# Kernel tuning notes

Measured on AMD Instinct MI355X. Metric: run time of the kernel, lower is better.

The kernel has to match this reference:

```python
import jax, jax.numpy as jnp
import numpy as np

N = 10000
E = 80000


def gat_layer(x, src, dst, W, a_src, a_dst, b):
    # x: [N, Fin], W: [Fin, Fout]
    xw = x @ W                              # [N, Fout]
    al_src = xw @ a_src                     # [N]
    al_dst = xw @ a_dst                     # [N]
    e = jax.nn.leaky_relu(al_src[src] + al_dst[dst], 0.2)  # [E+N]
    m = jax.lax.stop_gradient(jax.ops.segment_max(e, dst, num_segments=N))
    ex = jnp.exp(e - m[dst])
    denom = jax.ops.segment_sum(ex, dst, num_segments=N)
    alpha = ex / (denom[dst] + 1e-16)       # PyG softmax eps
    out = jax.ops.segment_sum(alpha[:, None] * xw[src], dst, num_segments=N)
    return out + b


def setup_inputs() -> dict:
    key = jax.random.key(0)
    ks = jax.random.split(key, 12)
    x = jax.random.normal(ks[0], (N, 256), dtype=jnp.float32)
    edge_index = jax.random.randint(ks[1], (2, E), 0, N, dtype=jnp.int64)
    def glorot(k, fi, fo):
        return jax.random.normal(k, (fi, fo), jnp.float32) * jnp.sqrt(2.0 / (fi + fo))
    W1 = glorot(ks[2], 256, 2048)
    W2 = glorot(ks[3], 2048, 2048)
    W3 = glorot(ks[4], 2048, 1024)
    a1s = jax.random.normal(ks[5], (2048,), jnp.float32) * 0.05
    a1d = jax.random.normal(ks[6], (2048,), jnp.float32) * 0.05
    a2s = jax.random.normal(ks[7], (2048,), jnp.float32) * 0.05
    a2d = jax.random.normal(ks[8], (2048,), jnp.float32) * 0.05
    a3s = jax.random.normal(ks[9], (1024,), jnp.float32) * 0.05
    a3d = jax.random.normal(ks[10], (1024,), jnp.float32) * 0.05
    b1 = jnp.zeros((2048,), jnp.float32)
    b2 = jnp.zeros((2048,), jnp.float32)
    b3 = jnp.zeros((1024,), jnp.float32)
    return {"x": x, "edge_index": edge_index, "W1": W1, "W2": W2, "W3": W3,
            "a1s": a1s, "a1d": a1d, "a2s": a2s, "a2d": a2d, "a3s": a3s, "a3d": a3d,
            "b1": b1, "b2": b2, "b3": b3}


def reference(x, edge_index, W1, W2, W3, a1s, a1d, a2s, a2d, a3s, a3d, b1, b2, b3):
    # add self loops (PyG GATConv default add_self_loops=True)
    loop = jnp.arange(N, dtype=edge_index.dtype)
    src = jnp.concatenate([edge_index[0], loop])
    dst = jnp.concatenate([edge_index[1], loop])
    h = jax.nn.relu(gat_layer(x, src, dst, W1, a1s, a1d, b1))
    h = jax.nn.relu(gat_layer(h, src, dst, W2, a2s, a2d, b2))
    h = jax.nn.relu(gat_layer(h, src, dst, W3, a3s, a3d, b3))
    # F.normalize(dim=1), eps=1e-12
    norm = jnp.linalg.norm(h, axis=1, keepdims=True)
    return h / jnp.maximum(norm, 1e-12)
```

## Files before the change

kernel.cpp:

```cpp
#include <hip/hip_runtime.h>
#include <hip/hip_bf16.h>
#include <math.h>


typedef __attribute__((ext_vector_type(8))) short short8;
typedef __attribute__((ext_vector_type(4))) float f32x4;

#define GLOAD_LDS16(g, l)                                            \
  __builtin_amdgcn_global_load_lds(                                  \
      (const __attribute__((address_space(1))) void*)(g),            \
      (__attribute__((address_space(3))) void*)(l), 16, 0, 0)

#define CFENCE asm volatile("" ::: "memory")

__device__ __forceinline__ float bf16_to_f32(ushort u) {
  return __uint_as_float(((unsigned int)u) << 16);
}

__device__ __forceinline__ float block_reduce_sum_bcast(float v) {
#pragma unroll
  for (int off = 32; off > 0; off >>= 1) v += __shfl_down(v, off, 64);
  __shared__ float tmp[4];
  __shared__ float res;
  int lane = threadIdx.x & 63, w = threadIdx.x >> 6;
  if (lane == 0) tmp[w] = v;
  __syncthreads();
  if (threadIdx.x == 0) res = tmp[0] + tmp[1] + tmp[2] + tmp[3];
  __syncthreads();
  float out = res;
  __syncthreads();
  return out;
}

__device__ __forceinline__ float block_reduce_max_bcast(float v) {
#pragma unroll
  for (int off = 32; off > 0; off >>= 1) v = fmaxf(v, __shfl_down(v, off, 64));
  __shared__ float tmpm[4];
  __shared__ float resm;
  int lane = threadIdx.x & 63, w = threadIdx.x >> 6;
  if (lane == 0) tmpm[w] = v;
  __syncthreads();
  if (threadIdx.x == 0) resm = fmaxf(fmaxf(tmpm[0], tmpm[1]), fmaxf(tmpm[2], tmpm[3]));
  __syncthreads();
  float out = resm;
  __syncthreads();
  return out;
}

__global__ void detect_kernel(const int* __restrict__ ei32, int* __restrict__ flag) {
  __shared__ int cnt;
  if (threadIdx.x == 0) cnt = 0;
  __syncthreads();
  int zeros = 0;
  for (int i = threadIdx.x; i < 1024; i += 256) {
    if (ei32[2 * i + 1] == 0) zeros++;
  }
  atomicAdd(&cnt, zeros);
  __syncthreads();
  if (threadIdx.x == 0) *flag = (cnt > 900) ? 1 : 0;
}

__global__ void convert_kernel(const void* __restrict__ ei, const int* __restrict__ flag,
                               int E, int* __restrict__ src, int* __restrict__ dst) {
  int i = blockIdx.x * blockDim.x + threadIdx.x;
  if (i >= E) return;
  if (*flag) {
    const long long* p = (const long long*)ei;
    src[i] = (int)p[i];
    dst[i] = (int)p[E + i];
  } else {
    const int* p = (const int*)ei;
    src[i] = p[i];
    dst[i] = p[E + i];
  }
}

__global__ __launch_bounds__(256) void convert_f32_bf16(const float* __restrict__ in,
                                                        __hip_bfloat16* __restrict__ out,
                                                        int n) {
  int i = blockIdx.x * blockDim.x + threadIdx.x;
  if (i < n) out[i] = __float2bfloat16(in[i]);
}

__global__ __launch_bounds__(256) void transpose_w(const float* __restrict__ W,
                                                   __hip_bfloat16* __restrict__ Wt,
                                                   int K, int Nout) {
  __shared__ float t[32][33];
  int tx = threadIdx.x & 31, ty = threadIdx.x >> 5;
  int n0 = blockIdx.x * 32, k0 = blockIdx.y * 32;
#pragma unroll
  for (int i = 0; i < 4; ++i) {
    int k = k0 + ty + i * 8;
    t[ty + i * 8][tx] = W[(size_t)k * Nout + n0 + tx];
  }
  __syncthreads();
#pragma unroll
  for (int i = 0; i < 4; ++i) {
    int n = n0 + ty + i * 8;
    Wt[(size_t)n * K + k0 + tx] = __float2bfloat16(t[tx][ty + i * 8]);
  }
}

__global__ __launch_bounds__(256) void matvec_wa(const float* __restrict__ W,
                                                 const float* __restrict__ a_s,
                                                 const float* __restrict__ a_d,
                                                 float* __restrict__ wa_s,
                                                 float* __restrict__ wa_d, int F) {
  int k = blockIdx.x;
  const float* row = W + (size_t)k * F;
  float s1 = 0.f, s2 = 0.f;
  for (int f = threadIdx.x; f < F; f += 256) {
    float w = row[f];
    s1 += w * a_s[f];
    s2 += w * a_d[f];
  }
  float r1 = block_reduce_sum_bcast(s1);
  float r2 = block_reduce_sum_bcast(s2);
  if (threadIdx.x == 0) {
    wa_s[k] = r1;
    wa_d[k] = r2;
  }
}

template <int FPT>
__global__ __launch_bounds__(256) void compute_al(const ushort* __restrict__ H,
                                                  const float* __restrict__ wa_s,
                                                  const float* __restrict__ wa_d,
                                                  float* __restrict__ als,
                                                  float* __restrict__ ald, int F) {
  int n = blockIdx.x;
  const ushort* row = H + (size_t)n * F;
  float s1 = 0.f, s2 = 0.f;
  if (FPT == 8) {
    int base = threadIdx.x * 8;
    short8 v = *(const short8*)(row + base);
#pragma unroll
    for (int j = 0; j < 8; ++j) {
      float f = bf16_to_f32((ushort)v[j]);
      s1 += f * wa_s[base + j];
      s2 += f * wa_d[base + j];
    }
  } else {
    float f = bf16_to_f32(row[threadIdx.x]);
    s1 = f * wa_s[threadIdx.x];
    s2 = f * wa_d[threadIdx.x];
  }
  float r1 = block_reduce_sum_bcast(s1);
  float r2 = block_reduce_sum_bcast(s2);
  if (threadIdx.x == 0) {
    als[n] = r1;
    ald[n] = r2;
  }
}

__global__ void count_kernel(const int* __restrict__ dst, int* __restrict__ counts, int E) {
  int i = blockIdx.x * blockDim.x + threadIdx.x;
  if (i < E) atomicAdd(&counts[dst[i]], 1);
}

__global__ __launch_bounds__(1024) void scan_kernel(const int* __restrict__ counts,
                                                    int* __restrict__ rowptr,
                                                    int* __restrict__ cursor, int Nn) {
  __shared__ int part[1024];
  int tid = threadIdx.x;
  int chunk = (Nn + 1023) / 1024;
  int base = tid * chunk;
  int s = 0;
  for (int i = 0; i < chunk; ++i) {
    int idx = base + i;
    if (idx < Nn) s += counts[idx];
  }
  part[tid] = s;
  __syncthreads();
  for (int off = 1; off < 1024; off <<= 1) {
    int v = 0;
    if (tid >= off) v = part[tid - off];
    __syncthreads();
    if (tid >= off) part[tid] += v;
    __syncthreads();
  }
  int run = (tid == 0) ? 0 : part[tid - 1];
  for (int i = 0; i < chunk; ++i) {
    int idx = base + i;
    if (idx < Nn) {
      rowptr[idx] = run;
      cursor[idx] = run;
      run += counts[idx];
    }
  }
  if (tid == 1023) rowptr[Nn] = part[1023];
}

__global__ void fill_kernel(const int* __restrict__ src, const int* __restrict__ dst,
                            int* __restrict__ cursor, int* __restrict__ eidx, int E) {
  int i = blockIdx.x * blockDim.x + threadIdx.x;
  if (i < E) {
    int pos = atomicAdd(&cursor[dst[i]], 1);
    eidx[pos] = src[i];
  }
}

template <int FPT>
__global__ __launch_bounds__(256) void aggregate(const ushort* __restrict__ H,
                                                 const float* __restrict__ als,
                                                 const float* __restrict__ ald,
                                                 const int* __restrict__ rowptr,
                                                 const int* __restrict__ eidx,
                                                 ushort* __restrict__ out, int F) {
  int n = blockIdx.x;
  int tid = threadIdx.x;
  int beg = rowptr[n], end = rowptr[n + 1];
  int deg = end - beg;
  float aldn = ald[n];

  float lm = -INFINITY;
  for (int j = tid; j < deg; j += 256) {
    int s = eidx[beg + j];
    float e = als[s] + aldn;
    e = (e > 0.f) ? e : 0.2f * e;
    lm = fmaxf(lm, e);
  }
  if (tid == 0) {
    float e = als[n] + aldn;
    e = (e > 0.f) ? e : 0.2f * e;
    lm = fmaxf(lm, e);
  }
  float m = block_reduce_max_bcast(lm);

  float ls = 0.f;
  for (int j = tid; j < deg; j += 256) {
    int s = eidx[beg + j];
    float e = als[s] + aldn;
    e = (e > 0.f) ? e : 0.2f * e;
    ls += expf(e - m);
  }
  if (tid == 0) {
    float e = als[n] + aldn;
    e = (e > 0.f) ? e : 0.2f * e;
    ls += expf(e - m);
  }
  float denom = block_reduce_sum_bcast(ls) + 1e-16f;
  float inv_denom = 1.f / denom;

  float acc[FPT];
#pragma unroll
  for (int i = 0; i < FPT; ++i) acc[i] = 0.f;

  __shared__ float alpha_sh[256];
  __shared__ int src_sh[256];
  int total = deg + 1;
  for (int c0 = 0; c0 < total; c0 += 256) {
    int j = c0 + tid;
    if (j < total) {
      int s = (j < deg) ? eidx[beg + j] : n;
      float e = als[s] + aldn;
      e = (e > 0.f) ? e : 0.2f * e;
      alpha_sh[tid] = expf(e - m) * inv_denom;
      src_sh[tid] = s;
    }
    __syncthreads();
    int cn = min(256, total - c0);
    for (int jj = 0; jj < cn; ++jj) {
      float al = alpha_sh[jj];
      const ushort* row = H + (size_t)src_sh[jj] * F;
      if (FPT == 1) {
        acc[0] += al * bf16_to_f32(row[tid]);
      } else {
#pragma unroll
        for (int i = 0; i < FPT / 2; ++i) {
          unsigned int u = *(const unsigned int*)(row + tid * 2 + i * 512);
          acc[2 * i]     += al * __uint_as_float((u & 0xffffu) << 16);
          acc[2 * i + 1] += al * __uint_as_float(u & 0xffff0000u);
        }
      }
    }
    __syncthreads();
  }

#pragma unroll
  for (int i = 0; i < FPT; ++i) {
    int col = (FPT == 1) ? tid : (tid * 2 + (i >> 1) * 512 + (i & 1));
    __hip_bfloat16 hv = __float2bfloat16(acc[i]);
    out[(size_t)n * F + col] = *(ushort*)&hv;
  }
}

template <bool BF16OUT>
__global__ __launch_bounds__(256, 4) void gemm_t128(const ushort* __restrict__ A,
                                                    const ushort* __restrict__ Bt,
                                                    const float* __restrict__ bias,
                                                    void* __restrict__ C,
                                                    int M, int K, int Nout) {
  constexpr int BUF = 8192;
  extern __shared__ ushort lds[];
  const int tid = threadIdx.x;
  const int l = tid & 63, w = tid >> 6;
  const int wm = w >> 1, wn = w & 1;
  const int l15 = l & 15, lhi = l >> 4;

  int nwg = gridDim.x * gridDim.y;
  int lin = blockIdx.y * gridDim.x + blockIdx.x;
  if ((nwg & 7) == 0) lin = (lin & 7) * (nwg >> 3) + (lin >> 3);
  const int bx = lin % gridDim.x, by = lin / gridDim.x;
  const int row0 = by * 128, col0 = bx * 128;

  const int c8sw = (l & 3) ^ (((l >> 5) & 1) << 1);
  const int lrow = l >> 2;
  const int chsw = lhi ^ (((l15 >> 3) & 1) << 1);
  const int rd_off = l15 * 32 + chsw * 8;

  const int sA0 = w * 2;
  const ushort* ga[2];
  const ushort* gb[2];
#pragma unroll
  for (int j = 0; j < 2; ++j) {
    int ar = min(row0 + (sA0 + j) * 16 + lrow, M - 1);
    ga[j] = A + (size_t)ar * K + c8sw * 8;
    gb[j] = Bt + (size_t)(col0 + (sA0 + j) * 16 + lrow) * K + c8sw * 8;
  }

#define STAGE(nb, kn)                                                     \
  do {                                                                    \
    GLOAD_LDS16(ga[0] + (kn), &lds[(nb)*BUF + (sA0 + 0) * 512]);          \
    GLOAD_LDS16(ga[1] + (kn), &lds[(nb)*BUF + (sA0 + 1) * 512]);          \
    GLOAD_LDS16(gb[0] + (kn), &lds[(nb)*BUF + 4096 + (sA0 + 0) * 512]);   \
    GLOAD_LDS16(gb[1] + (kn), &lds[(nb)*BUF + 4096 + (sA0 + 1) * 512]);   \
  } while (0)

  f32x4 acc[4][4] = {};

#define PHASE(cur, WAITLIT, STAGE_STMT)                                              \
  do {                                                                               \
    STAGE_STMT;                                                                      \
    asm volatile("s_waitcnt vmcnt(" WAITLIT ")" ::: "memory");                       \
    __builtin_amdgcn_s_barrier();                                                    \
    CFENCE;                                                                          \
    short8 af[4], bf[4];                                                             \
    const ushort* Ab = &lds[(cur)*BUF];                                              \
    const ushort* Bb = &lds[(cur)*BUF + 4096];                                       \
    _Pragma("unroll") for (int m = 0; m < 4; ++m)                                    \
        af[m] = *(const short8*)(Ab + (wm * 4 + m) * 512 + rd_off);                  \
    _Pragma("unroll") for (int n = 0; n < 4; ++n)                                    \
        bf[n] = *(const short8*)(Bb + (wn * 4 + n) * 512 + rd_off);                  \
    __builtin_amdgcn_s_setprio(1);                                                   \
    _Pragma("unroll") for (int m = 0; m < 4; ++m)                                    \
        _Pragma("unroll") for (int n = 0; n < 4; ++n)                                \
            acc[m][n] = __builtin_amdgcn_mfma_f32_16x16x32_bf16(                     \
                af[m], bf[n], acc[m][n], 0, 0, 0);                                   \
    __builtin_amdgcn_s_setprio(0);                                                   \
    CFENCE;                                                                          \
    __builtin_amdgcn_s_barrier();                                                    \
    CFENCE;                                                                          \
  } while (0)

  const int nt = K >> 5;
  STAGE(0, 0);

  int cur = 0;
  for (int t = 0; t < nt - 1; ++t) {
    const int kn = (t + 1) << 5;
    PHASE(cur, "4", STAGE(cur ^ 1, kn));
    cur ^= 1;
  }
  PHASE(cur, "0", );

#pragma unroll
  for (int mi = 0; mi < 4; ++mi) {
#pragma unroll
    for (int v = 0; v < 4; ++v) {
      int r = row0 + wm * 64 + mi * 16 + lhi * 4 + v;
      if (r < M) {
#pragma unroll
        for (int n = 0; n < 4; ++n) {
          int col = col0 + wn * 64 + n * 16 + l15;
          float val = fmaxf(acc[mi][n][v] + bias[col], 0.f);
          size_t idx = (size_t)r * Nout + col;
          if (BF16OUT)
            ((__hip_bfloat16*)C)[idx] = __float2bfloat16(val);
          else
            ((float*)C)[idx] = val;
        }
      }
    }
  }
#undef PHASE
#undef STAGE
}

__global__ __launch_bounds__(256) void normalize_kernel(const float* __restrict__ h,
                                                        float* __restrict__ out,
                                                        int F) {
  int n = blockIdx.x;
  const float* row = h + (size_t)n * F;
  float ss = 0.f;
  for (int f = threadIdx.x; f < F; f += 256) {
    float v = row[f];
    ss += v * v;
  }
  float tot = block_reduce_sum_bcast(ss);
  float inv = 1.f / fmaxf(sqrtf(tot), 1e-12f);
  for (int f = threadIdx.x; f < F; f += 256) {
    out[(size_t)n * F + f] = row[f] * inv;
  }
}

extern "C" void kernel_launch(void* const* d_in, const int* in_sizes, int n_in,
                              void* d_out, int out_size, void* d_ws, size_t ws_size,
                              hipStream_t stream) {
  const float* x   = (const float*)d_in[0];
  const void*  ei  = d_in[1];
  const float* W1  = (const float*)d_in[2];
  const float* W2  = (const float*)d_in[3];
  const float* W3  = (const float*)d_in[4];
  const float* a1s = (const float*)d_in[5];
  const float* a1d = (const float*)d_in[6];
  const float* a2s = (const float*)d_in[7];
  const float* a2d = (const float*)d_in[8];
  const float* a3s = (const float*)d_in[9];
  const float* a3d = (const float*)d_in[10];
  const float* b1  = (const float*)d_in[11];
  const float* b2  = (const float*)d_in[12];
  const float* b3  = (const float*)d_in[13];

  const int N = in_sizes[0] / 256;
  const int E = in_sizes[1] / 2;

  char* ws = (char*)d_ws;
  size_t off = 0;
  auto alloc = [&](size_t bytes) -> void* {
    void* p = ws + off;
    off += (bytes + 255) & ~(size_t)255;
    return p;
  };
  ushort* h    = (ushort*)alloc((size_t)N * 2048 * 2);
  ushort* hagg = (ushort*)alloc((size_t)N * 2048 * 2);
  float* hf32  = (float*)alloc((size_t)N * 1024 * 4);
  ushort* xb   = (ushort*)alloc((size_t)N * 256 * 2);
  __hip_bfloat16* Wt1 = (__hip_bfloat16*)alloc((size_t)2048 * 256 * 2);
  __hip_bfloat16* Wt2 = (__hip_bfloat16*)alloc((size_t)2048 * 2048 * 2);
  __hip_bfloat16* Wt3 = (__hip_bfloat16*)alloc((size_t)1024 * 2048 * 2);
  float* wa1s = (float*)alloc(256 * 4);
  float* wa1d = (float*)alloc(256 * 4);
  float* wa2s = (float*)alloc(2048 * 4);
  float* wa2d = (float*)alloc(2048 * 4);
  float* wa3s = (float*)alloc(2048 * 4);
  float* wa3d = (float*)alloc(2048 * 4);
  float* als   = (float*)alloc((size_t)N * 4);
  float* ald   = (float*)alloc((size_t)N * 4);
  int* counts  = (int*)alloc((size_t)N * 4);
  int* rowptr  = (int*)alloc((size_t)(N + 1) * 4);
  int* cursor  = (int*)alloc((size_t)N * 4);
  int* eidx    = (int*)alloc((size_t)E * 4);
  int* src32   = (int*)alloc((size_t)E * 4);
  int* dst32   = (int*)alloc((size_t)E * 4);
  int* flag    = (int*)alloc(256);

  hipFuncSetAttribute((const void*)gemm_t128<true>,
                      hipFuncAttributeMaxDynamicSharedMemorySize, 32768);
  hipFuncSetAttribute((const void*)gemm_t128<false>,
                      hipFuncAttributeMaxDynamicSharedMemorySize, 32768);

  detect_kernel<<<1, 256, 0, stream>>>((const int*)ei, flag);
  convert_kernel<<<(E + 255) / 256, 256, 0, stream>>>(ei, flag, E, src32, dst32);
  hipMemsetAsync(counts, 0, (size_t)N * 4, stream);
  count_kernel<<<(E + 255) / 256, 256, 0, stream>>>(dst32, counts, E);
  scan_kernel<<<1, 1024, 0, stream>>>(counts, rowptr, cursor, N);
  fill_kernel<<<(E + 255) / 256, 256, 0, stream>>>(src32, dst32, cursor, eidx, E);

  convert_f32_bf16<<<(N * 256 + 255) / 256, 256, 0, stream>>>(x, (__hip_bfloat16*)xb, N * 256);
  transpose_w<<<dim3(2048 / 32, 256 / 32), 256, 0, stream>>>(W1, Wt1, 256, 2048);
  transpose_w<<<dim3(2048 / 32, 2048 / 32), 256, 0, stream>>>(W2, Wt2, 2048, 2048);
  transpose_w<<<dim3(1024 / 32, 2048 / 32), 256, 0, stream>>>(W3, Wt3, 2048, 1024);
  matvec_wa<<<256, 256, 0, stream>>>(W1, a1s, a1d, wa1s, wa1d, 2048);
  matvec_wa<<<2048, 256, 0, stream>>>(W2, a2s, a2d, wa2s, wa2d, 2048);
  matvec_wa<<<2048, 256, 0, stream>>>(W3, a3s, a3d, wa3s, wa3d, 1024);

  dim3 blk(256);
  int mb = (N + 127) / 128;

  compute_al<1><<<N, blk, 0, stream>>>(xb, wa1s, wa1d, als, ald, 256);
  aggregate<1><<<N, blk, 0, stream>>>(xb, als, ald, rowptr, eidx, hagg, 256);
  gemm_t128<true><<<dim3(2048 / 128, mb), blk, 32768, stream>>>(hagg, (const ushort*)Wt1, b1, h, N, 256, 2048);

  compute_al<8><<<N, blk, 0, stream>>>(h, wa2s, wa2d, als, ald, 2048);
  aggregate<8><<<N, blk, 0, stream>>>(h, als, ald, rowptr, eidx, hagg, 2048);
  gemm_t128<true><<<dim3(2048 / 128, mb), blk, 32768, stream>>>(hagg, (const ushort*)Wt2, b2, h, N, 2048, 2048);

  compute_al<8><<<N, blk, 0, stream>>>(h, wa3s, wa3d, als, ald, 2048);
  aggregate<8><<<N, blk, 0, stream>>>(h, als, ald, rowptr, eidx, hagg, 2048);
  gemm_t128<false><<<dim3(1024 / 128, mb), blk, 32768, stream>>>(hagg, (const ushort*)Wt3, b3, hf32, N, 2048, 1024);

  normalize_kernel<<<N, blk, 0, stream>>>(hf32, (float*)d_out, 1024);
}
```

Measured before the change: 428.7 us.

## Fuse attention logits and row sum-of-squares into GEMM epilogues, drop index conversion

The next layer's attention scalars (h·wa_s, h·wa_d) are now computed in the GEMM epilogue through a 16-lane shuffle reduction plus atomicAdd, which removes the separate compute_al passes over the 2048-wide bf16 activations. The final GEMM likewise accumulates per-row sums of squares, so normalization no longer re-reads each row to reduce it. The edge-index detection and conversion kernels are removed and the input is read directly as int32, assuming that layout. This adds atomics and a memset, and the epilogue sums fp32 values before bf16 rounding, so results differ slightly from the old path.

```diff
diff --git a/kernel.cpp b/kernel.cpp
--- a/kernel.cpp
+++ b/kernel.cpp
@@ -45,34 +45,6 @@
   float out = resm;
   __syncthreads();
   return out;
-}
-
-__global__ void detect_kernel(const int* __restrict__ ei32, int* __restrict__ flag) {
-  __shared__ int cnt;
-  if (threadIdx.x == 0) cnt = 0;
-  __syncthreads();
-  int zeros = 0;
-  for (int i = threadIdx.x; i < 1024; i += 256) {
-    if (ei32[2 * i + 1] == 0) zeros++;
-  }
-  atomicAdd(&cnt, zeros);
-  __syncthreads();
-  if (threadIdx.x == 0) *flag = (cnt > 900) ? 1 : 0;
-}
-
-__global__ void convert_kernel(const void* __restrict__ ei, const int* __restrict__ flag,
-                               int E, int* __restrict__ src, int* __restrict__ dst) {
-  int i = blockIdx.x * blockDim.x + threadIdx.x;
-  if (i >= E) return;
-  if (*flag) {
-    const long long* p = (const long long*)ei;
-    src[i] = (int)p[i];
-    dst[i] = (int)p[E + i];
-  } else {
-    const int* p = (const int*)ei;
-    src[i] = p[i];
-    dst[i] = p[E + i];
-  }
 }
 
 __global__ __launch_bounds__(256) void convert_f32_bf16(const float* __restrict__ in,
@@ -122,29 +94,16 @@
   }
 }
 
-template <int FPT>
-__global__ __launch_bounds__(256) void compute_al(const ushort* __restrict__ H,
-                                                  const float* __restrict__ wa_s,
-                                                  const float* __restrict__ wa_d,
-                                                  float* __restrict__ als,
-                                                  float* __restrict__ ald, int F) {
+__global__ __launch_bounds__(256) void compute_al1(const ushort* __restrict__ H,
+                                                   const float* __restrict__ wa_s,
+                                                   const float* __restrict__ wa_d,
+                                                   float* __restrict__ als,
+                                                   float* __restrict__ ald) {
   int n = blockIdx.x;
-  const ushort* row = H + (size_t)n * F;
-  float s1 = 0.f, s2 = 0.f;
-  if (FPT == 8) {
-    int base = threadIdx.x * 8;
-    short8 v = *(const short8*)(row + base);
-#pragma unroll
-    for (int j = 0; j < 8; ++j) {
-      float f = bf16_to_f32((ushort)v[j]);
-      s1 += f * wa_s[base + j];
-      s2 += f * wa_d[base + j];
-    }
-  } else {
-    float f = bf16_to_f32(row[threadIdx.x]);
-    s1 = f * wa_s[threadIdx.x];
-    s2 = f * wa_d[threadIdx.x];
-  }
+  const ushort* row = H + (size_t)n * 256;
+  float f = bf16_to_f32(row[threadIdx.x]);
+  float s1 = f * wa_s[threadIdx.x];
+  float s2 = f * wa_d[threadIdx.x];
   float r1 = block_reduce_sum_bcast(s1);
   float r2 = block_reduce_sum_bcast(s2);
   if (threadIdx.x == 0) {
@@ -285,11 +244,15 @@
   }
 }
 
-template <bool BF16OUT>
+template <bool BF16OUT, int EPI>
 __global__ __launch_bounds__(256, 4) void gemm_t128(const ushort* __restrict__ A,
                                                     const ushort* __restrict__ Bt,
                                                     const float* __restrict__ bias,
                                                     void* __restrict__ C,
+                                                    const float* __restrict__ wa_s,
+                                                    const float* __restrict__ wa_d,
+                                                    float* __restrict__ aux1,
+                                                    float* __restrict__ aux2,
                                                     int M, int K, int Nout) {
   constexpr int BUF = 8192;
   extern __shared__ ushort lds[];
@@ -369,36 +332,53 @@
 #pragma unroll
     for (int v = 0; v < 4; ++v) {
       int r = row0 + wm * 64 + mi * 16 + lhi * 4 + v;
-      if (r < M) {
-#pragma unroll
-        for (int n = 0; n < 4; ++n) {
-          int col = col0 + wn * 64 + n * 16 + l15;
-          float val = fmaxf(acc[mi][n][v] + bias[col], 0.f);
+      bool rin = (r < M);
+      float pS = 0.f, pD = 0.f;
+#pragma unroll
+      for (int n = 0; n < 4; ++n) {
+        int col = col0 + wn * 64 + n * 16 + l15;
+        float val = fmaxf(acc[mi][n][v] + bias[col], 0.f);
+        if (rin) {
           size_t idx = (size_t)r * Nout + col;
           if (BF16OUT)
             ((__hip_bfloat16*)C)[idx] = __float2bfloat16(val);
           else
             ((float*)C)[idx] = val;
+          if (EPI == 1) {
+            pS += val * wa_s[col];
+            pD += val * wa_d[col];
+          } else if (EPI == 2) {
+            pS += val * val;
+          }
         }
       }
+      if (EPI == 1) {
+#pragma unroll
+        for (int off = 1; off < 16; off <<= 1) {
+          pS += __shfl_xor(pS, off, 64);
+          pD += __shfl_xor(pD, off, 64);
+        }
+        if (l15 == 0 && rin) {
+          atomicAdd(&aux1[r], pS);
+          atomicAdd(&aux2[r], pD);
+        }
+      } else if (EPI == 2) {
+#pragma unroll
+        for (int off = 1; off < 16; off <<= 1) pS += __shfl_xor(pS, off, 64);
+        if (l15 == 0 && rin) atomicAdd(&aux1[r], pS);
+      }
     }
   }
 #undef PHASE
 #undef STAGE
 }
 
-__global__ __launch_bounds__(256) void normalize_kernel(const float* __restrict__ h,
-                                                        float* __restrict__ out,
-                                                        int F) {
+__global__ __launch_bounds__(256) void normalize_ss(const float* __restrict__ h,
+                                                    const float* __restrict__ ss,
+                                                    float* __restrict__ out, int F) {
   int n = blockIdx.x;
+  float inv = 1.f / fmaxf(sqrtf(ss[n]), 1e-12f);
   const float* row = h + (size_t)n * F;
-  float ss = 0.f;
-  for (int f = threadIdx.x; f < F; f += 256) {
-    float v = row[f];
-    ss += v * v;
-  }
-  float tot = block_reduce_sum_bcast(ss);
-  float inv = 1.f / fmaxf(sqrtf(tot), 1e-12f);
   for (int f = threadIdx.x; f < F; f += 256) {
     out[(size_t)n * F + f] = row[f] * inv;
   }
@@ -408,7 +388,7 @@
                               void* d_out, int out_size, void* d_ws, size_t ws_size,
                               hipStream_t stream) {
   const float* x   = (const float*)d_in[0];
-  const void*  ei  = d_in[1];
+  const int*   ei  = (const int*)d_in[1];
   const float* W1  = (const float*)d_in[2];
   const float* W2  = (const float*)d_in[3];
   const float* W3  = (const float*)d_in[4];
@@ -445,27 +425,33 @@
   float* wa2d = (float*)alloc(2048 * 4);
   float* wa3s = (float*)alloc(2048 * 4);
   float* wa3d = (float*)alloc(2048 * 4);
-  float* als   = (float*)alloc((size_t)N * 4);
-  float* ald   = (float*)alloc((size_t)N * 4);
+  float* als1 = (float*)alloc((size_t)N * 4);
+  float* ald1 = (float*)alloc((size_t)N * 4);
+  float* alaux = (float*)alloc((size_t)N * 5 * 4);
+  float* als2 = alaux;
+  float* ald2 = alaux + N;
+  float* als3 = alaux + 2 * (size_t)N;
+  float* ald3 = alaux + 3 * (size_t)N;
+  float* ssq  = alaux + 4 * (size_t)N;
   int* counts  = (int*)alloc((size_t)N * 4);
   int* rowptr  = (int*)alloc((size_t)(N + 1) * 4);
   int* cursor  = (int*)alloc((size_t)N * 4);
   int* eidx    = (int*)alloc((size_t)E * 4);
-  int* src32   = (int*)alloc((size_t)E * 4);
-  int* dst32   = (int*)alloc((size_t)E * 4);
-  int* flag    = (int*)alloc(256);
-
-  hipFuncSetAttribute((const void*)gemm_t128<true>,
+
+  const int* srcp = ei;
+  const int* dstp = ei + E;
+
+  hipFuncSetAttribute((const void*)gemm_t128<true, 1>,
                       hipFuncAttributeMaxDynamicSharedMemorySize, 32768);
-  hipFuncSetAttribute((const void*)gemm_t128<false>,
+  hipFuncSetAttribute((const void*)gemm_t128<false, 2>,
                       hipFuncAttributeMaxDynamicSharedMemorySize, 32768);
 
-  detect_kernel<<<1, 256, 0, stream>>>((const int*)ei, flag);
-  convert_kernel<<<(E + 255) / 256, 256, 0, stream>>>(ei, flag, E, src32, dst32);
+  hipMemsetAsync(alaux, 0, (size_t)N * 5 * 4, stream);
   hipMemsetAsync(counts, 0, (size_t)N * 4, stream);
-  count_kernel<<<(E + 255) / 256, 256, 0, stream>>>(dst32, counts, E);
+
+  count_kernel<<<(E + 255) / 256, 256, 0, stream>>>(dstp, counts, E);
   scan_kernel<<<1, 1024, 0, stream>>>(counts, rowptr, cursor, N);
-  fill_kernel<<<(E + 255) / 256, 256, 0, stream>>>(src32, dst32, cursor, eidx, E);
+  fill_kernel<<<(E + 255) / 256, 256, 0, stream>>>(srcp, dstp, cursor, eidx, E);
 
   convert_f32_bf16<<<(N * 256 + 255) / 256, 256, 0, stream>>>(x, (__hip_bfloat16*)xb, N * 256);
   transpose_w<<<dim3(2048 / 32, 256 / 32), 256, 0, stream>>>(W1, Wt1, 256, 2048);
@@ -478,17 +464,18 @@
   dim3 blk(256);
   int mb = (N + 127) / 128;
 
-  compute_al<1><<<N, blk, 0, stream>>>(xb, wa1s, wa1d, als, ald, 256);
-  aggregate<1><<<N, blk, 0, stream>>>(xb, als, ald, rowptr, eidx, hagg, 256);
-  gemm_t128<true><<<dim3(2048 / 128, mb), blk, 32768, stream>>>(hagg, (const ushort*)Wt1, b1, h, N, 256, 2048);
-
-  compute_al<8><<<N, blk, 0, stream>>>(h, wa2s, wa2d, als, ald, 2048);
-  aggregate<8><<<N, blk, 0, stream>>>(h, als, ald, rowptr, eidx, hagg, 2048);
-  gemm_t128<true><<<dim3(2048 / 128, mb), blk, 32768, stream>>>(hagg, (const ushort*)Wt2, b2, h, N, 2048, 2048);
-
-  compute_al<8><<<N, blk, 0, stream>>>(h, wa3s, wa3d, als, ald, 2048);
-  aggregate<8><<<N, blk, 0, stream>>>(h, als, ald, rowptr, eidx, hagg, 2048);
-  gemm_t128<false><<<dim3(1024 / 128, mb), blk, 32768, stream>>>(hagg, (const ushort*)Wt3, b3, hf32, N, 2048, 1024);
-
-  normalize_kernel<<<N, blk, 0, stream>>>(hf32, (float*)d_out, 1024);
-}
+  compute_al1<<<N, blk, 0, stream>>>(xb, wa1s, wa1d, als1, ald1);
+  aggregate<1><<<N, blk, 0, stream>>>(xb, als1, ald1, rowptr, eidx, hagg, 256);
+  gemm_t128<true, 1><<<dim3(16, mb), blk, 32768, stream>>>(
+      hagg, (const ushort*)Wt1, b1, h, wa2s, wa2d, als2, ald2, N, 256, 2048);
+
+  aggregate<8><<<N, blk, 0, stream>>>(h, als2, ald2, rowptr, eidx, hagg, 2048);
+  gemm_t128<true, 1><<<dim3(16, mb), blk, 32768, stream>>>(
+      hagg, (const ushort*)Wt2, b2, h, wa3s, wa3d, als3, ald3, N, 2048, 2048);
+
+  aggregate<8><<<N, blk, 0, stream>>>(h, als3, ald3, rowptr, eidx, hagg, 2048);
+  gemm_t128<false, 2><<<dim3(8, mb), blk, 32768, stream>>>(
+      hagg, (const ushort*)Wt3, b3, hf32, nullptr, nullptr, ssq, nullptr, N, 2048, 1024);
+
+  normalize_ss<<<N, blk, 0, stream>>>(hf32, ssq, (float*)d_out, 1024);
+}
```

Result: slower. 470.6 us (+9.8%).
